# Performance work log

Hardware: AMD Instinct MI355X
Metric: run time of the kernel (lower is better)

Reference implementation:

```python
import jax, jax.numpy as jnp
import numpy as np


def setup_inputs() -> dict:
    key = jax.random.key(0)
    ks = jax.random.split(key, 16)
    H, F, W, Hh, C = 8, 256, 96, 96, 64
    inp = {
        "X": jax.random.normal(ks[0], (F, W, Hh), jnp.float32),
        "WQ_task": jax.random.uniform(ks[1], (H, F, 1, 1), jnp.float32),
        "BQ_task": jax.random.uniform(ks[2], (H, F, 1, 1), jnp.float32),
        "WK_task": jax.random.uniform(ks[3], (F, 1, 1), jnp.float32),
        "BK_task": jax.random.uniform(ks[4], (F, 1, 1), jnp.float32),
        "WV_task": jax.random.uniform(ks[5], (C, 1, 1), jnp.float32),
        "BV_task": jax.random.uniform(ks[6], (C, 1, 1), jnp.float32),
        "WQ_t_minus_1": jax.random.uniform(ks[7], (H, F, 1, 1), jnp.float32),
        "WQ_x": jax.random.uniform(ks[8], (1, F, 1, 1), jnp.float32),
        "BQ": jax.random.uniform(ks[9], (H, F, 1, 1), jnp.float32),
        "WK_x": jax.random.uniform(ks[10], (F, 1, 1), jnp.float32),
        "BK": jax.random.uniform(ks[11], (F, 1, 1), jnp.float32),
        "prev_Q": jax.random.normal(ks[12], (H, F, W, Hh), jnp.float32),
        "Vconv_w": jax.random.normal(ks[13], (C, F, 3, 3), jnp.float32) * 0.02,
        "Vconv_b": jnp.zeros((C,), jnp.float32),
    }
    return inp


def reference(X, WQ_task, BQ_task, WK_task, BK_task, WV_task, BV_task,
              WQ_t_minus_1, WQ_x, BQ, WK_x, BK, prev_Q, Vconv_w, Vconv_b):
    F, W, Hh = X.shape
    C = Vconv_w.shape[0]
    rX = X[None]  # (1, F, W, Hh)

    # Q: (n_heads, F, W, Hh); K: (F, W, Hh)
    Q = WQ_task * (WQ_t_minus_1 * prev_Q + WQ_x * rX + BQ) + BQ_task
    K = WK_task * (WK_x * X + BK) + BK_task

    # Original: similarity = sum over [head, feature] of Q[n,f,w,h] * K[f,v,u]
    # (K is broadcast over heads) == dot(Q.sum(heads), K) over features.
    Qs = Q.sum(axis=0)  # (F, W, Hh)
    sim = jnp.einsum('fwh,fvu->whvu', Qs, K).reshape(W, Hh, W * Hh)
    attn = jax.nn.softmax(sim, axis=-1)  # softmax over flattened key positions

    # V: 3x3 same conv F -> C, then task affine
    V = jax.lax.conv_general_dilated(
        rX, Vconv_w, window_strides=(1, 1), padding='SAME',
        dimension_numbers=('NCHW', 'OIHW', 'NCHW'))
    V = (WV_task * (V[0] + Vconv_b[:, None, None]) + BV_task).reshape(C, W * Hh)

    # out[c, w, h] = sum_k attn[w, h, k] * V[c, k]
    out = jnp.einsum('whk,ck->cwh', attn, V)
    return out
```

## Files before the change

### kernel.cpp

```cpp
#include <hip/hip_runtime.h>
#include <hip/hip_fp16.h>

#define S 9216
#define F 256
#define W 96
#define HH 96
#define C 64
#define NH 8
#define KSPLIT 8
#define KV_PER_SPLIT (S / KSPLIT)
#define KTILE 64
#define NKT (KV_PER_SPLIT / KTILE)

typedef _Float16 half8 __attribute__((ext_vector_type(8)));
typedef float floatx4 __attribute__((ext_vector_type(4)));


__global__ __launch_bounds__(256) void rowmean_kernel(
    const float* __restrict__ prevQ, const float* __restrict__ Xg,
    float* __restrict__ pqmean, float* __restrict__ xmean) {
  int row = blockIdx.x;
  const float* src = (row < 2048) ? (prevQ + (size_t)row * S)
                                  : (Xg + (size_t)(row - 2048) * S);
  float s = 0.f;
  for (int i = threadIdx.x; i < S; i += 256) s += src[i];
  __shared__ float red[256];
  red[threadIdx.x] = s;
  __syncthreads();
  for (int off = 128; off > 0; off >>= 1) {
    if ((int)threadIdx.x < off) red[threadIdx.x] += red[threadIdx.x + off];
    __syncthreads();
  }
  if (threadIdx.x == 0) {
    float m = red[0] * (1.f / (float)S);
    if (row < 2048) pqmean[row] = m; else xmean[row - 2048] = m;
  }
}

__global__ __launch_bounds__(256) void coef_kernel(
    const float* __restrict__ WQ_task, const float* __restrict__ BQ_task,
    const float* __restrict__ WK_task, const float* __restrict__ BK_task,
    const float* __restrict__ WQ_tm1, const float* __restrict__ WQ_x,
    const float* __restrict__ BQ, const float* __restrict__ WK_x,
    const float* __restrict__ BK, const float* __restrict__ pqmean,
    const float* __restrict__ xmean,
    float* __restrict__ qscale, float* __restrict__ c1, float* __restrict__ c0,
    float* __restrict__ kw, float* __restrict__ kb,
    float* __restrict__ qbar, float* __restrict__ kbar) {
  int f = threadIdx.x;
  float sumW = 0.f, sc0 = 0.f, qb = 0.f;
  for (int n = 0; n < NH; n++) {
    float wq = WQ_task[n * F + f];
    float qs = wq * WQ_tm1[n * F + f];
    qscale[f * NH + n] = qs;
    sumW += wq;
    sc0 += wq * BQ[n * F + f] + BQ_task[n * F + f];
    qb += qs * pqmean[n * F + f];
  }
  float c1v = WQ_x[f] * sumW;
  c1[f] = c1v; c0[f] = sc0;
  float kwv = WK_task[f] * WK_x[f];
  float kbv = WK_task[f] * BK[f] + BK_task[f];
  kw[f] = kwv; kb[f] = kbv;
  qbar[f] = qb + c1v * xmean[f] + sc0;
  kbar[f] = kwv * xmean[f] + kbv;
}

__global__ __launch_bounds__(256) void prep_kernel(
    const float* __restrict__ Xg, const float* __restrict__ prevQ,
    const float* __restrict__ qscale, const float* __restrict__ c1,
    const float* __restrict__ c0, const float* __restrict__ kw,
    const float* __restrict__ kb, const float* __restrict__ qbar,
    const float* __restrict__ kbar,
    _Float16* __restrict__ Qf, _Float16* __restrict__ Kf,
    float* __restrict__ rowK) {
  __shared__ float qt[32][33];
  __shared__ float kt[32][33];
  __shared__ float rk[8][32];
  int tx = threadIdx.x & 31, ty = threadIdx.x >> 5;
  int s0 = blockIdx.x * 32, f0 = blockIdx.y * 32;
  int s = s0 + tx;
  float rkacc = 0.f;
  for (int fi = ty; fi < 32; fi += 8) {
    int f = f0 + fi;
    float x = Xg[(size_t)f * S + s];
    float q = c1[f] * x + c0[f];
    #pragma unroll
    for (int n = 0; n < NH; n++)
      q += qscale[f * NH + n] * prevQ[((size_t)n * F + f) * S + s];
    q -= qbar[f];
    float k = kw[f] * x + kb[f] - kbar[f];
    qt[fi][tx] = q;
    kt[fi][tx] = k;
    rkacc += qbar[f] * k;
  }
  rk[ty][tx] = rkacc;
  __syncthreads();
  {
    int t = threadIdx.x;
    int isK = t >> 7;
    int tt = t & 127;
    int s_sub = tt >> 2, lw = tt & 3;
    half8 h;
    #pragma unroll
    for (int jj = 0; jj < 8; jj++) {
      float v = isK ? kt[lw * 8 + jj][s_sub] : qt[lw * 8 + jj][s_sub];
      h[jj] = (_Float16)v;
    }
    size_t fi = (size_t)((s0 + s_sub) >> 4) * 8 + (f0 >> 5);
    int lane = (s_sub & 15) + 16 * lw;
    half8* dst = (half8*)(isK ? Kf : Qf);
    dst[fi * 64 + lane] = h;
  }
  if (ty == 0) {
    float t = 0.f;
    #pragma unroll
    for (int i = 0; i < 8; i++) t += rk[i][tx];
    atomicAdd(&rowK[s], t);
  }
}

__global__ __launch_bounds__(256) void conv_kernel(
    const float* __restrict__ Xg, const float* __restrict__ Wc,
    const float* __restrict__ bias, const float* __restrict__ WV_task,
    const float* __restrict__ BV_task, _Float16* __restrict__ Vf) {
  __shared__ float wlds[4 * 2304];
  int c0 = blockIdx.y * 4;
  for (int i = threadIdx.x; i < 4 * 2304; i += 256)
    wlds[i] = Wc[(size_t)c0 * 2304 + i];
  __syncthreads();
  int p = blockIdx.x * 256 + threadIdx.x;
  int w = p / HH, h = p % HH;
  float acc0 = 0.f, acc1 = 0.f, acc2 = 0.f, acc3 = 0.f;
  for (int f = 0; f < F; f++) {
    const float* xp = Xg + (size_t)f * S;
    float xv[9];
    #pragma unroll
    for (int ky = 0; ky < 3; ky++) {
      int ww = w + ky - 1;
      #pragma unroll
      for (int kx = 0; kx < 3; kx++) {
        int hh = h + kx - 1;
        xv[ky * 3 + kx] = (ww >= 0 && ww < W && hh >= 0 && hh < HH)
                              ? xp[ww * HH + hh] : 0.f;
      }
    }
    const float* wl = wlds + f * 9;
    #pragma unroll
    for (int t = 0; t < 9; t++) {
      float x = xv[t];
      acc0 += x * wl[t];
      acc1 += x * wl[2304 + t];
      acc2 += x * wl[2 * 2304 + t];
      acc3 += x * wl[3 * 2304 + t];
    }
  }
  float accs[4] = {acc0, acc1, acc2, acc3};
  int k = p;
  #pragma unroll
  for (int cc = 0; cc < 4; cc++) {
    int c = c0 + cc;
    float v = WV_task[c] * (accs[cc] + bias[c]) + BV_task[c];
    size_t idx = (((size_t)(k >> 5) * 4 + (c >> 4)) * 64 +
                  ((c & 15) + 16 * ((k & 31) >> 3))) * 8 + (k & 7);
    Vf[idx] = (_Float16)v;
  }
}

__global__ __launch_bounds__(256, 2) void flash_kernel(
    const _Float16* __restrict__ Qf, const _Float16* __restrict__ Kf,
    const _Float16* __restrict__ Vf, const float* __restrict__ rowK,
    float* __restrict__ out_part, float* __restrict__ m_part,
    float* __restrict__ l_part) {
  int qt = blockIdx.x, sp = blockIdx.y;
  int wave = threadIdx.x >> 6, lane = threadIdx.x & 63;
  int q0 = qt * 64 + wave * 16;
  int lr = lane & 15, lhi = lane >> 4;
  __shared__ __align__(16) _Float16 plds[4][16][72];

  half8 qfrag[8];
  {
    const half8* qb = (const half8*)Qf + ((size_t)(q0 >> 4) * 8) * 64 + lane;
    #pragma unroll
    for (int ch = 0; ch < 8; ch++) qfrag[ch] = qb[ch * 64];
  }

  floatx4 oacc[4] = {};
  float m_run[4], l_run[4];
  #pragma unroll
  for (int j = 0; j < 4; j++) { m_run[j] = -1e30f; l_run[j] = 0.f; }

  for (int kt = 0; kt < NKT; kt++) {
    int k0 = sp * KV_PER_SPLIT + kt * KTILE;
    const half8* kfb = (const half8*)Kf + (size_t)(k0 >> 4) * 512 + lane;
    half8 bf[4][8];
    #pragma unroll
    for (int ks = 0; ks < 4; ks++)
      #pragma unroll
      for (int ch = 0; ch < 8; ch++) bf[ks][ch] = kfb[ks * 512 + ch * 64];
    float rk4[4];
    #pragma unroll
    for (int ks = 0; ks < 4; ks++) rk4[ks] = rowK[k0 + ks * 16 + lr];

    floatx4 sacc[4] = {};
    #pragma unroll
    for (int ch = 0; ch < 8; ch++)
      #pragma unroll
      for (int ks = 0; ks < 4; ks++)
        sacc[ks] = __builtin_amdgcn_mfma_f32_16x16x32_f16(qfrag[ch], bf[ks][ch],
                                                          sacc[ks], 0, 0, 0);

    const half8* vfb = (const half8*)Vf + (size_t)(k0 >> 5) * 256 + lane;
    half8 vf[2][4];
    #pragma unroll
    for (int kc = 0; kc < 2; kc++)
      #pragma unroll
      for (int cs = 0; cs < 4; cs++) vf[kc][cs] = vfb[kc * 256 + cs * 64];

    float tmax[4];
    #pragma unroll
    for (int j = 0; j < 4; j++) tmax[j] = -1e30f;
    #pragma unroll
    for (int ks = 0; ks < 4; ks++) {
      #pragma unroll
      for (int j = 0; j < 4; j++) {
        sacc[ks][j] += rk4[ks];
        tmax[j] = fmaxf(tmax[j], sacc[ks][j]);
      }
    }
    #pragma unroll
    for (int off = 1; off < 16; off <<= 1)
      #pragma unroll
      for (int j = 0; j < 4; j++)
        tmax[j] = fmaxf(tmax[j], __shfl_xor(tmax[j], off, 64));

    float ef[4], rsum[4];
    #pragma unroll
    for (int j = 0; j < 4; j++) {
      float mn = fmaxf(m_run[j], tmax[j]);
      ef[j] = __expf(m_run[j] - mn);
      m_run[j] = mn;
      rsum[j] = 0.f;
    }
    #pragma unroll
    for (int ks = 0; ks < 4; ks++) {
      #pragma unroll
      for (int j = 0; j < 4; j++) {
        float p = __expf(sacc[ks][j] - m_run[j]);
        rsum[j] += p;
        plds[wave][lhi * 4 + j][ks * 16 + lr] = (_Float16)p;
      }
    }
    #pragma unroll
    for (int off = 1; off < 16; off <<= 1)
      #pragma unroll
      for (int j = 0; j < 4; j++) rsum[j] += __shfl_xor(rsum[j], off, 64);
    #pragma unroll
    for (int j = 0; j < 4; j++) l_run[j] = l_run[j] * ef[j] + rsum[j];
    #pragma unroll
    for (int cs = 0; cs < 4; cs++)
      #pragma unroll
      for (int j = 0; j < 4; j++) oacc[cs][j] *= ef[j];

    #pragma unroll
    for (int kc = 0; kc < 2; kc++) {
      half8 pfrag = *(const half8*)(&plds[wave][lr][kc * 32 + lhi * 8]);
      #pragma unroll
      for (int cs = 0; cs < 4; cs++)
        oacc[cs] = __builtin_amdgcn_mfma_f32_16x16x32_f16(pfrag, vf[kc][cs],
                                                          oacc[cs], 0, 0, 0);
    }
  }

  size_t base = (size_t)sp * S + q0;
  #pragma unroll
  for (int cs = 0; cs < 4; cs++)
    #pragma unroll
    for (int j = 0; j < 4; j++)
      out_part[(base + lhi * 4 + j) * C + cs * 16 + lr] = oacc[cs][j];
  if (lr == 0) {
    #pragma unroll
    for (int j = 0; j < 4; j++) {
      m_part[base + lhi * 4 + j] = m_run[j];
      l_part[base + lhi * 4 + j] = l_run[j];
    }
  }
}

__global__ __launch_bounds__(256) void combine_kernel(
    const float* __restrict__ out_part, const float* __restrict__ m_part,
    const float* __restrict__ l_part, float* __restrict__ out) {
  int q = blockIdx.x * 4 + (threadIdx.x >> 6);
  int c = threadIdx.x & 63;
  float m = -1e30f;
  #pragma unroll
  for (int i = 0; i < KSPLIT; i++) m = fmaxf(m, m_part[(size_t)i * S + q]);
  float l = 0.f, acc = 0.f;
  #pragma unroll
  for (int i = 0; i < KSPLIT; i++) {
    float wgt = __expf(m_part[(size_t)i * S + q] - m);
    l += wgt * l_part[(size_t)i * S + q];
    acc += wgt * out_part[((size_t)i * S + q) * C + c];
  }
  out[(size_t)c * S + q] = acc / l;
}

extern "C" void kernel_launch(void* const* d_in, const int* in_sizes, int n_in,
                              void* d_out, int out_size, void* d_ws,
                              size_t ws_size, hipStream_t stream) {
  const float* Xg      = (const float*)d_in[0];
  const float* WQ_task = (const float*)d_in[1];
  const float* BQ_task = (const float*)d_in[2];
  const float* WK_task = (const float*)d_in[3];
  const float* BK_task = (const float*)d_in[4];
  const float* WV_task = (const float*)d_in[5];
  const float* BV_task = (const float*)d_in[6];
  const float* WQ_tm1  = (const float*)d_in[7];
  const float* WQ_x    = (const float*)d_in[8];
  const float* BQ      = (const float*)d_in[9];
  const float* WK_x    = (const float*)d_in[10];
  const float* BK      = (const float*)d_in[11];
  const float* prevQ   = (const float*)d_in[12];
  const float* Wc      = (const float*)d_in[13];
  const float* bias    = (const float*)d_in[14];
  float* out = (float*)d_out;

  char* ws = (char*)d_ws;
  size_t off = 0;
  auto alloc = [&](size_t bytes) {
    void* p = ws + off;
    off += (bytes + 255) & ~(size_t)255;
    return p;
  };
  _Float16* Qf   = (_Float16*)alloc((size_t)S * F * 2);
  _Float16* Kf   = (_Float16*)alloc((size_t)S * F * 2);
  _Float16* Vf   = (_Float16*)alloc((size_t)C * S * 2);
  float* rowK    = (float*)alloc((size_t)S * 4);
  float* pqmean  = (float*)alloc(2048 * 4);
  float* xmean   = (float*)alloc(256 * 4);
  float* qscale  = (float*)alloc(256 * 8 * 4);
  float* c1      = (float*)alloc(256 * 4);
  float* c0      = (float*)alloc(256 * 4);
  float* kw      = (float*)alloc(256 * 4);
  float* kb      = (float*)alloc(256 * 4);
  float* qbar    = (float*)alloc(256 * 4);
  float* kbar    = (float*)alloc(256 * 4);
  float* out_part = (float*)alloc((size_t)KSPLIT * S * C * 4);
  float* m_part   = (float*)alloc((size_t)KSPLIT * S * 4);
  float* l_part   = (float*)alloc((size_t)KSPLIT * S * 4);

  hipMemsetAsync(rowK, 0, (size_t)S * 4, stream);

  rowmean_kernel<<<2304, 256, 0, stream>>>(prevQ, Xg, pqmean, xmean);
  coef_kernel<<<1, 256, 0, stream>>>(WQ_task, BQ_task, WK_task, BK_task,
                                     WQ_tm1, WQ_x, BQ, WK_x, BK, pqmean, xmean,
                                     qscale, c1, c0, kw, kb, qbar, kbar);
  prep_kernel<<<dim3(S / 32, F / 32), 256, 0, stream>>>(
      Xg, prevQ, qscale, c1, c0, kw, kb, qbar, kbar, Qf, Kf, rowK);
  conv_kernel<<<dim3(S / 256, C / 4), 256, 0, stream>>>(Xg, Wc, bias, WV_task,
                                                        BV_task, Vf);
  flash_kernel<<<dim3(S / 64, KSPLIT), 256, 0, stream>>>(
      Qf, Kf, Vf, rowK, out_part, m_part, l_part);
  combine_kernel<<<S / 4, 256, 0, stream>>>(out_part, m_part, l_part, out);
}
```

Baseline: 510.5 us.

## Stage K/V tiles in LDS and process two query subtiles per wave

Result: slower. 535.5 us (+4.9%).

```diff
diff --git a/kernel.cpp b/kernel.cpp
--- a/kernel.cpp
+++ b/kernel.cpp
@@ -20,10 +20,14 @@
     const float* __restrict__ prevQ, const float* __restrict__ Xg,
     float* __restrict__ pqmean, float* __restrict__ xmean) {
   int row = blockIdx.x;
-  const float* src = (row < 2048) ? (prevQ + (size_t)row * S)
-                                  : (Xg + (size_t)(row - 2048) * S);
+  const float4* src = (const float4*)((row < 2048) ? (prevQ + (size_t)row * S)
+                                                   : (Xg + (size_t)(row - 2048) * S));
   float s = 0.f;
-  for (int i = threadIdx.x; i < S; i += 256) s += src[i];
+  #pragma unroll
+  for (int j = 0; j < 9; j++) {
+    float4 v = src[j * 256 + threadIdx.x];
+    s += v.x + v.y + v.z + v.w;
+  }
   __shared__ float red[256];
   red[threadIdx.x] = s;
   __syncthreads();
@@ -174,115 +178,134 @@
     float* __restrict__ l_part) {
   int qt = blockIdx.x, sp = blockIdx.y;
   int wave = threadIdx.x >> 6, lane = threadIdx.x & 63;
-  int q0 = qt * 64 + wave * 16;
   int lr = lane & 15, lhi = lane >> 4;
+  __shared__ __align__(16) _Float16 kvbuf[2560 * 8];
   __shared__ __align__(16) _Float16 plds[4][16][72];
-
-  half8 qfrag[8];
+  half8* ldsv = (half8*)kvbuf;
+
+  half8 qfrag[2][8];
   {
-    const half8* qb = (const half8*)Qf + ((size_t)(q0 >> 4) * 8) * 64 + lane;
-    #pragma unroll
-    for (int ch = 0; ch < 8; ch++) qfrag[ch] = qb[ch * 64];
-  }
-
-  floatx4 oacc[4] = {};
-  float m_run[4], l_run[4];
-  #pragma unroll
-  for (int j = 0; j < 4; j++) { m_run[j] = -1e30f; l_run[j] = 0.f; }
+    const half8* qb = (const half8*)Qf;
+    #pragma unroll
+    for (int qs = 0; qs < 2; qs++) {
+      size_t t16 = (size_t)(qt * 8 + wave * 2 + qs) * 8;
+      #pragma unroll
+      for (int ch = 0; ch < 8; ch++) qfrag[qs][ch] = qb[(t16 + ch) * 64 + lane];
+    }
+  }
+
+  floatx4 oacc[2][4] = {};
+  float m_run[2][4], l_run[2][4];
+  #pragma unroll
+  for (int qs = 0; qs < 2; qs++)
+    #pragma unroll
+    for (int j = 0; j < 4; j++) { m_run[qs][j] = -1e30f; l_run[qs][j] = 0.f; }
 
   for (int kt = 0; kt < NKT; kt++) {
     int k0 = sp * KV_PER_SPLIT + kt * KTILE;
-    const half8* kfb = (const half8*)Kf + (size_t)(k0 >> 4) * 512 + lane;
-    half8 bf[4][8];
-    #pragma unroll
-    for (int ks = 0; ks < 4; ks++)
-      #pragma unroll
-      for (int ch = 0; ch < 8; ch++) bf[ks][ch] = kfb[ks * 512 + ch * 64];
+    const half8* ksrc = (const half8*)Kf + (size_t)(k0 >> 4) * 512;
+    const half8* vsrc = (const half8*)Vf + (size_t)(k0 >> 5) * 256;
+    __syncthreads();
+    #pragma unroll
+    for (int j = 0; j < 10; j++) {
+      int idx = j * 256 + (int)threadIdx.x;
+      const half8* src = (idx < 2048) ? (ksrc + idx) : (vsrc + (idx - 2048));
+      ldsv[idx] = *src;
+    }
+    __syncthreads();
+
     float rk4[4];
     #pragma unroll
     for (int ks = 0; ks < 4; ks++) rk4[ks] = rowK[k0 + ks * 16 + lr];
 
-    floatx4 sacc[4] = {};
-    #pragma unroll
-    for (int ch = 0; ch < 8; ch++)
-      #pragma unroll
-      for (int ks = 0; ks < 4; ks++)
-        sacc[ks] = __builtin_amdgcn_mfma_f32_16x16x32_f16(qfrag[ch], bf[ks][ch],
-                                                          sacc[ks], 0, 0, 0);
-
-    const half8* vfb = (const half8*)Vf + (size_t)(k0 >> 5) * 256 + lane;
-    half8 vf[2][4];
-    #pragma unroll
-    for (int kc = 0; kc < 2; kc++)
-      #pragma unroll
-      for (int cs = 0; cs < 4; cs++) vf[kc][cs] = vfb[kc * 256 + cs * 64];
-
-    float tmax[4];
-    #pragma unroll
-    for (int j = 0; j < 4; j++) tmax[j] = -1e30f;
-    #pragma unroll
-    for (int ks = 0; ks < 4; ks++) {
+    floatx4 sacc[2][4] = {};
+    #pragma unroll
+    for (int ch = 0; ch < 8; ch++) {
+      #pragma unroll
+      for (int ks = 0; ks < 4; ks++) {
+        half8 kf = ldsv[(ks * 8 + ch) * 64 + lane];
+        sacc[0][ks] = __builtin_amdgcn_mfma_f32_16x16x32_f16(qfrag[0][ch], kf,
+                                                             sacc[0][ks], 0, 0, 0);
+        sacc[1][ks] = __builtin_amdgcn_mfma_f32_16x16x32_f16(qfrag[1][ch], kf,
+                                                             sacc[1][ks], 0, 0, 0);
+      }
+    }
+
+    #pragma unroll
+    for (int qs = 0; qs < 2; qs++) {
+      float tmax[4];
+      #pragma unroll
+      for (int j = 0; j < 4; j++) tmax[j] = -1e30f;
+      #pragma unroll
+      for (int ks = 0; ks < 4; ks++) {
+        #pragma unroll
+        for (int j = 0; j < 4; j++) {
+          sacc[qs][ks][j] += rk4[ks];
+          tmax[j] = fmaxf(tmax[j], sacc[qs][ks][j]);
+        }
+      }
+      #pragma unroll
+      for (int off = 1; off < 16; off <<= 1)
+        #pragma unroll
+        for (int j = 0; j < 4; j++)
+          tmax[j] = fmaxf(tmax[j], __shfl_xor(tmax[j], off, 64));
+
+      float ef[4], rsum[4];
       #pragma unroll
       for (int j = 0; j < 4; j++) {
-        sacc[ks][j] += rk4[ks];
-        tmax[j] = fmaxf(tmax[j], sacc[ks][j]);
-      }
-    }
-    #pragma unroll
-    for (int off = 1; off < 16; off <<= 1)
+        float mn = fmaxf(m_run[qs][j], tmax[j]);
+        ef[j] = __expf(m_run[qs][j] - mn);
+        m_run[qs][j] = mn;
+        rsum[j] = 0.f;
+      }
+      #pragma unroll
+      for (int ks = 0; ks < 4; ks++) {
+        #pragma unroll
+        for (int j = 0; j < 4; j++) {
+          float p = __expf(sacc[qs][ks][j] - m_run[qs][j]);
+          rsum[j] += p;
+          plds[wave][lhi * 4 + j][ks * 16 + lr] = (_Float16)p;
+        }
+      }
+      #pragma unroll
+      for (int off = 1; off < 16; off <<= 1)
+        #pragma unroll
+        for (int j = 0; j < 4; j++) rsum[j] += __shfl_xor(rsum[j], off, 64);
       #pragma unroll
       for (int j = 0; j < 4; j++)
-        tmax[j] = fmaxf(tmax[j], __shfl_xor(tmax[j], off, 64));
-
-    float ef[4], rsum[4];
-    #pragma unroll
-    for (int j = 0; j < 4; j++) {
-      float mn = fmaxf(m_run[j], tmax[j]);
-      ef[j] = __expf(m_run[j] - mn);
-      m_run[j] = mn;
-      rsum[j] = 0.f;
-    }
-    #pragma unroll
-    for (int ks = 0; ks < 4; ks++) {
+        l_run[qs][j] = l_run[qs][j] * ef[j] + rsum[j];
+      #pragma unroll
+      for (int cs = 0; cs < 4; cs++)
+        #pragma unroll
+        for (int j = 0; j < 4; j++) oacc[qs][cs][j] *= ef[j];
+
+      #pragma unroll
+      for (int kc = 0; kc < 2; kc++) {
+        half8 pfrag = *(const half8*)(&plds[wave][lr][kc * 32 + lhi * 8]);
+        #pragma unroll
+        for (int cs = 0; cs < 4; cs++) {
+          half8 vfrag = ldsv[2048 + (kc * 4 + cs) * 64 + lane];
+          oacc[qs][cs] = __builtin_amdgcn_mfma_f32_16x16x32_f16(pfrag, vfrag,
+                                                                oacc[qs][cs], 0, 0, 0);
+        }
+      }
+    }
+  }
+
+  #pragma unroll
+  for (int qs = 0; qs < 2; qs++) {
+    size_t base = (size_t)sp * S + qt * 128 + wave * 32 + qs * 16;
+    #pragma unroll
+    for (int cs = 0; cs < 4; cs++)
+      #pragma unroll
+      for (int j = 0; j < 4; j++)
+        out_part[(base + lhi * 4 + j) * C + cs * 16 + lr] = oacc[qs][cs][j];
+    if (lr == 0) {
       #pragma unroll
       for (int j = 0; j < 4; j++) {
-        float p = __expf(sacc[ks][j] - m_run[j]);
-        rsum[j] += p;
-        plds[wave][lhi * 4 + j][ks * 16 + lr] = (_Float16)p;
-      }
-    }
-    #pragma unroll
-    for (int off = 1; off < 16; off <<= 1)
-      #pragma unroll
-      for (int j = 0; j < 4; j++) rsum[j] += __shfl_xor(rsum[j], off, 64);
-    #pragma unroll
-    for (int j = 0; j < 4; j++) l_run[j] = l_run[j] * ef[j] + rsum[j];
-    #pragma unroll
-    for (int cs = 0; cs < 4; cs++)
-      #pragma unroll
-      for (int j = 0; j < 4; j++) oacc[cs][j] *= ef[j];
-
-    #pragma unroll
-    for (int kc = 0; kc < 2; kc++) {
-      half8 pfrag = *(const half8*)(&plds[wave][lr][kc * 32 + lhi * 8]);
-      #pragma unroll
-      for (int cs = 0; cs < 4; cs++)
-        oacc[cs] = __builtin_amdgcn_mfma_f32_16x16x32_f16(pfrag, vf[kc][cs],
-                                                          oacc[cs], 0, 0, 0);
-    }
-  }
-
-  size_t base = (size_t)sp * S + q0;
-  #pragma unroll
-  for (int cs = 0; cs < 4; cs++)
-    #pragma unroll
-    for (int j = 0; j < 4; j++)
-      out_part[(base + lhi * 4 + j) * C + cs * 16 + lr] = oacc[cs][j];
-  if (lr == 0) {
-    #pragma unroll
-    for (int j = 0; j < 4; j++) {
-      m_part[base + lhi * 4 + j] = m_run[j];
-      l_part[base + lhi * 4 + j] = l_run[j];
+        m_part[base + lhi * 4 + j] = m_run[qs][j];
+        l_part[base + lhi * 4 + j] = l_run[qs][j];
+      }
     }
   }
 }
@@ -359,7 +382,7 @@
       Xg, prevQ, qscale, c1, c0, kw, kb, qbar, kbar, Qf, Kf, rowK);
   conv_kernel<<<dim3(S / 256, C / 4), 256, 0, stream>>>(Xg, Wc, bias, WV_task,
                                                         BV_task, Vf);
-  flash_kernel<<<dim3(S / 64, KSPLIT), 256, 0, stream>>>(
+  flash_kernel<<<dim3(S / 128, KSPLIT), 256, 0, stream>>>(
       Qf, Kf, Vf, rowK, out_part, m_part, l_part);
   combine_kernel<<<S / 4, 256, 0, stream>>>(out_part, m_part, l_part, out);
 }
```
